# Kernel optimization log

Hardware: AMD Instinct MI355X
Metric: run time of the kernel (lower is better)

Reference implementation:

```python
import jax, jax.numpy as jnp
import numpy as np

B, L, D, N, H = 4, 1024, 1024, 16, 64  # batch, seq, d_model, n_head, d_head
R = 2 * L  # relative position table length
EPS = 1e-5


def setup_inputs() -> dict:
    key = jax.random.key(0)
    ks = jax.random.split(key, 16)
    s = D ** -0.5
    q = jax.random.normal(ks[0], (B, L, D), jnp.float32)
    k = jax.random.normal(ks[1], (B, L, D), jnp.float32)
    v = jax.random.normal(ks[2], (B, L, D), jnp.float32)
    pos_encodings = jax.random.normal(ks[3], (R, D), jnp.float32)
    padding = jax.random.randint(ks[4], (B, 1, 1, L), 0, 2).astype(bool)
    q_w = jax.random.normal(ks[5], (D, N, H), jnp.float32) * s
    k_w = jax.random.normal(ks[6], (D, N, H), jnp.float32) * s
    k_b = jnp.zeros((N, H), jnp.float32)
    v_w = jax.random.normal(ks[7], (D, N, H), jnp.float32) * s
    v_b = jnp.zeros((N, H), jnp.float32)
    r_w_bias = jax.random.normal(ks[8], (N, 1, H), jnp.float32) * 0.02
    r_r_bias = jax.random.normal(ks[9], (N, 1, H), jnp.float32) * 0.02
    r_kernel = jax.random.normal(ks[10], (N, D, H), jnp.float32) * s
    post_w = jax.random.normal(ks[11], (N, H, D), jnp.float32) * (N * H) ** -0.5
    post_b = jnp.zeros((D,), jnp.float32)
    ln_g = jnp.ones((D,), jnp.float32)
    ln_b = jnp.zeros((D,), jnp.float32)
    return dict(q=q, k=k, v=v, pos_encodings=pos_encodings, padding=padding,
                q_w=q_w, k_w=k_w, k_b=k_b, v_w=v_w, v_b=v_b,
                r_w_bias=r_w_bias, r_r_bias=r_r_bias, r_kernel=r_kernel,
                post_w=post_w, post_b=post_b, ln_g=ln_g, ln_b=ln_b)


def _funnel_attention(q, k, v, pos_encodings, padding, q_w, k_w, k_b, v_w, v_b,
                      r_w_bias, r_r_bias, r_kernel, post_w, post_b, ln_g, ln_b):
    input_q = q
    d_head = q_w.shape[-1]
    scale = d_head ** -0.5
    # head projections, laid out [b, n, l, h]
    qh = jnp.einsum('bld,dnh->bnlh', q, q_w)
    kh = jnp.einsum('bld,dnh->bnlh', k, k_w) + k_b[None, :, None, :]
    vh = jnp.einsum('bld,dnh->bnlh', v, v_w) + v_b[None, :, None, :]
    # content term with r_w_bias
    attn_score = jnp.einsum('bnlh,bnmh->bnlm', qh + r_w_bias[None], kh) * scale
    # relative-position term (rel_shift)
    r = jnp.einsum('rd,ndh->nrh', pos_encodings, r_kernel)  # [n, R, h]
    pos = jnp.einsum('bnlh,nrh->bnlr', qh + r_r_bias[None], r) * scale  # [b,n,L,R]
    b, n, q_len, r_len = pos.shape
    k_len = kh.shape[-2]
    shift = 1 + (q_len != k_len)
    pos = pos.reshape(b, n, r_len, q_len)
    pos = pos[:, :, shift:, :]
    pos = pos.reshape(b, n, q_len, r_len - shift)[..., :k_len]
    attn_score = attn_score + pos
    # key padding mask
    attn_score = attn_score - 1e6 * padding.astype(attn_score.dtype)
    attn_dist = jax.nn.softmax(attn_score, axis=-1)
    out = jnp.einsum('bnlm,bnmh->bnlh', attn_dist, vh)
    attn_out = jnp.einsum('bnlh,nhd->bld', out, post_w) + post_b
    x = input_q + attn_out
    mu = jnp.mean(x, axis=-1, keepdims=True)
    var = jnp.mean(jnp.square(x - mu), axis=-1, keepdims=True)
    return (x - mu) * jax.lax.rsqrt(var + EPS) * ln_g + ln_b


def reference(q, k, v, pos_encodings, padding, q_w, k_w, k_b, v_w, v_b,
              r_w_bias, r_r_bias, r_kernel, post_w, post_b, ln_g, ln_b):
    return _funnel_attention(q, k, v, pos_encodings, padding, q_w, k_w, k_b,
                             v_w, v_b, r_w_bias, r_r_bias, r_kernel,
                             post_w, post_b, ln_g, ln_b)
```

## Files before the change

### kernel.cpp

```cpp
#include <hip/hip_runtime.h>
#include <hip/hip_bf16.h>

#define Bb 4
#define Ls 1024
#define Dd 1024
#define Nn 16
#define Hh 64
#define Rr 2048

typedef __attribute__((ext_vector_type(8))) short short8;
typedef __attribute__((ext_vector_type(4))) short short4v;
typedef __attribute__((ext_vector_type(4))) float f32x4;

__device__ __forceinline__ float bf2f(short s) {
    union { unsigned u; float f; } c;
    c.u = ((unsigned)(unsigned short)s) << 16;
    return c.f;
}
__device__ __forceinline__ short f2bf(float f) {
    __hip_bfloat16 h = __float2bfloat16(f);
    return *reinterpret_cast<short*>(&h);
}

__device__ __forceinline__ void gld16(const void* g, void* l) {
    __builtin_amdgcn_global_load_lds(
        (const __attribute__((address_space(1))) unsigned int*)g,
        (__attribute__((address_space(3))) unsigned int*)l, 16, 0, 0);
}

struct CopyDesc {
    const float* src[4];
    short* dst[4];
    int n[4];
};

__global__ __launch_bounds__(256) void f2bf_multi(CopyDesc cd) {
    const int z = blockIdx.y;
    const int base = (blockIdx.x * 256 + threadIdx.x) * 8;
    if (base >= cd.n[z]) return;
    const float* s = cd.src[z] + base;
    const float4 a = *(const float4*)s;
    const float4 b = *(const float4*)(s + 4);
    short8 o;
    o[0] = f2bf(a.x); o[1] = f2bf(a.y); o[2] = f2bf(a.z); o[3] = f2bf(a.w);
    o[4] = f2bf(b.x); o[5] = f2bf(b.y); o[6] = f2bf(b.z); o[7] = f2bf(b.w);
    *(short8*)(cd.dst[z] + base) = o;
}

struct TransDesc {
    const float* src[4];
    short* dst[4];
};

__global__ __launch_bounds__(256) void transpose_all(
    TransDesc td, const float* __restrict__ rker, short* __restrict__ rkT)
{
    const int z = blockIdx.z;
    const float* in; short* out; int C, R;
    if (z < 4) {
        in = td.src[z]; out = td.dst[z]; C = 1024; R = 1024;
    } else {
        if (blockIdx.x != 0) return;
        in  = rker + (long)(z - 4) * 1024 * 64;
        out = rkT  + (long)(z - 4) * 64 * 1024;
        C = 64; R = 1024;
    }
    const int r0 = blockIdx.y * 64, c0 = blockIdx.x * 64;
    __shared__ float T[64][65];
    const int t = threadIdx.x;
    const int rr = t >> 4, c4 = (t & 15) * 4;
#pragma unroll
    for (int p = 0; p < 4; ++p) {
        const float4 v = *(const float4*)&in[(long)(r0 + p * 16 + rr) * C + c0 + c4];
        T[p * 16 + rr][c4 + 0] = v.x;
        T[p * 16 + rr][c4 + 1] = v.y;
        T[p * 16 + rr][c4 + 2] = v.z;
        T[p * 16 + rr][c4 + 3] = v.w;
    }
    __syncthreads();
#pragma unroll
    for (int p = 0; p < 4; ++p) {
        const int j = p * 16 + (t >> 4);
        const int d4 = (t & 15) * 4;
        short4v o;
#pragma unroll
        for (int u = 0; u < 4; ++u) o[u] = f2bf(T[d4 + u][j]);
        *(short4v*)&out[(long)(c0 + j) * R + r0 + d4] = o;
    }
}

__global__ __launch_bounds__(256) void gemm_bt(
    const short* __restrict__ A, int lda, long aStride,
    const short* __restrict__ Bt, int ldb, long bStride,
    const float* __restrict__ bias,
    const float* __restrict__ kb, const float* __restrict__ vb,
    const float* __restrict__ residual, int ldr,
    void* __restrict__ Cv, int ldc, long cStride, int out_bf16, int K, int zsplit)
{
    const int bid   = (int)blockIdx.x;
    const int chunk = (int)gridDim.x >> 3;
    const int work  = (bid & 7) * chunk + (bid >> 3);
    int z, r;
    if (work < zsplit) { z = work >> 8; r = work & 255; }
    else               { z = 3;         r = work - zsplit; }
    const int by = r >> 3;
    const int bx = r & 7;

    A  += (long)z * aStride;
    Bt += (long)z * bStride;

    const int row0 = by * 128;
    const int col0 = bx * 128;

    __shared__ short As[128 * 32];
    __shared__ short Bs[128 * 32];

    const int tid  = threadIdx.x;
    const int w    = tid >> 6;
    const int lane = tid & 63;
    const int quad = lane >> 4;
    const int ln16 = lane & 15;
    const int wr   = (w >> 1) * 64;
    const int wc   = (w & 1) * 64;

    f32x4 acc[4][4];
#pragma unroll
    for (int a = 0; a < 4; ++a)
#pragma unroll
        for (int b = 0; b < 4; ++b) acc[a][b] = (f32x4){0.f, 0.f, 0.f, 0.f};

    const int srow = w * 16 + (lane >> 2);
    const int scol = (lane & 3) * 8;
    const short* gA = A  + (long)(row0 + srow) * lda + scol;
    const short* gB = Bt + (long)(col0 + srow) * ldb + scol;
    short* lA0 = As + w * 512;
    short* lB0 = Bs + w * 512;

    for (int k0 = 0; k0 < K; k0 += 32) {
        __syncthreads();
        gld16(gA + k0,                  lA0);
        gld16(gA + k0 + (long)64 * lda, lA0 + 2048);
        gld16(gB + k0,                  lB0);
        gld16(gB + k0 + (long)64 * ldb, lB0 + 2048);
        __syncthreads();

        short8 af[4], bfr[4];
#pragma unroll
        for (int tm = 0; tm < 4; ++tm)
            af[tm] = *(const short8*)&As[(wr + tm * 16 + ln16) * 32 + quad * 8];
#pragma unroll
        for (int tn = 0; tn < 4; ++tn)
            bfr[tn] = *(const short8*)&Bs[(wc + tn * 16 + ln16) * 32 + quad * 8];
#pragma unroll
        for (int tm = 0; tm < 4; ++tm)
#pragma unroll
            for (int tn = 0; tn < 4; ++tn)
                acc[tm][tn] = __builtin_amdgcn_mfma_f32_16x16x32_bf16(
                    af[tm], bfr[tn], acc[tm][tn], 0, 0, 0);
    }

    const float* bz = bias;
    if (z == 1) bz = kb;
    else if (z == 2) bz = vb;

    float bv[4];
#pragma unroll
    for (int tn = 0; tn < 4; ++tn)
        bv[tn] = bz ? bz[col0 + wc + tn * 16 + ln16] : 0.f;

    short* Cb = (short*)Cv + (long)z * cStride;
    float* Cf = (float*)Cv + (long)z * cStride;
#pragma unroll
    for (int tm = 0; tm < 4; ++tm) {
#pragma unroll
        for (int r2 = 0; r2 < 4; ++r2) {
            const long row = row0 + wr + tm * 16 + quad * 4 + r2;
#pragma unroll
            for (int tn = 0; tn < 4; ++tn) {
                const int col = col0 + wc + tn * 16 + ln16;
                float val = acc[tm][tn][r2] + bv[tn];
                if (residual) val += residual[row * (long)ldr + col];
                if (out_bf16) Cb[row * (long)ldc + col] = f2bf(val);
                else          Cf[row * (long)ldc + col] = val;
            }
        }
    }
}

#define SCALE_L2E 0.18033688f

__global__ __launch_bounds__(256, 2) void attn_mfma(
    const short* __restrict__ qh, const short* __restrict__ kh,
    const short* __restrict__ vh, const short* __restrict__ rS,
    const int* __restrict__ padding, const float* __restrict__ rwb,
    const float* __restrict__ rrb, short* __restrict__ ao)
{
    const int bid   = (int)blockIdx.x;
    const int chunk = (int)gridDim.x >> 3;
    const int work  = (bid & 7) * chunk + (bid >> 3);
    const int lt = work & 7;
    const int n  = (work >> 3) & 15;
    const int b  = work >> 7;

    const int l0 = lt * 128;
    const int tid  = threadIdx.x;
    const int w    = tid >> 6;
    const int lane = tid & 63;
    const int quad = lane >> 4;
    const int ln16 = lane & 15;
    const int qb   = w * 32;

    __shared__ __align__(16) short ks[64 * 64];
    __shared__ __align__(16) short rsb[192 * 64];
    __shared__ __align__(16) short vsT[64][72];
    __shared__ __align__(16) short psm[4][16][72];
    __shared__ float padsAll[Ls];

    for (int i = tid; i < Ls; i += 256) {
        const float mask = -1.0e6f * (float)padding[b * Ls + i];
        padsAll[i] = (mask - 16.0f) * 1.44269504f;
    }

    short8 qwf[2][2], qrf[2][2];
#pragma unroll
    for (int qt = 0; qt < 2; ++qt) {
        const long rowoff =
            ((long)(b * Ls + l0 + qb + qt * 16 + ln16)) * (Nn * Hh) + n * Hh;
#pragma unroll
        for (int c = 0; c < 2; ++c) {
            const int kb2 = c * 32 + quad * 8;
            short8 qv = *(const short8*)(qh + rowoff + kb2);
#pragma unroll
            for (int j = 0; j < 8; ++j) {
                float qf = bf2f(qv[j]);
                qwf[qt][c][j] = f2bf(qf + rwb[n * Hh + kb2 + j]);
                qrf[qt][c][j] = f2bf(qf + rrb[n * Hh + kb2 + j]);
            }
        }
    }

    float lsum[2][4];
    f32x4 accO[2][4];
#pragma unroll
    for (int qt = 0; qt < 2; ++qt)
#pragma unroll
        for (int r = 0; r < 4; ++r) {
            lsum[qt][r] = 0.f;
            accO[qt][r] = (f32x4){0.f, 0.f, 0.f, 0.f};
        }

    const int srow8 = lane >> 3;
    const int sunit = (lane & 7) ^ srow8;
    const int swz   = ln16 & 7;

    const int kp = tid & 31, cq = (tid >> 5) * 8;
    short8 va, vb2;
    {
        const short* vp = vh + ((long)(b * Ls + 2 * kp)) * 1024 + n * 64 + cq;
        va  = *(const short8*)vp;
        vb2 = *(const short8*)(vp + 1024);
    }

    for (int mt = 0; mt < Ls / 64; ++mt) {
        const int m0 = mt * 64;
        __syncthreads();

#pragma unroll
        for (int j = 0; j < 2; ++j) {
            const int c = w * 2 + j;
            gld16(kh + ((long)(b * Ls + m0 + c * 8 + srow8)) * 1024
                     + n * 64 + sunit * 8,
                  ks + c * 512);
        }
        {
            const int blockBase = 897 + m0 - l0;
#pragma unroll
            for (int j = 0; j < 6; ++j) {
                const int c = w * 6 + j;
                int rg = blockBase + c * 8 + srow8;
                rg = rg < 2047 ? rg : 2047;
                gld16(rS + (long)rg * 1024 + n * 64 + sunit * 8,
                      rsb + c * 512);
            }
        }
#pragma unroll
        for (int u = 0; u < 8; ++u) {
            unsigned pk = ((unsigned)(unsigned short)va[u]) |
                          (((unsigned)(unsigned short)vb2[u]) << 16);
            *(unsigned*)&vsT[cq + u][2 * kp] = pk;
        }
        __syncthreads();

        {
            const int mn = (m0 + 64) & (Ls - 1);
            const short* vp = vh + ((long)(b * Ls + mn + 2 * kp)) * 1024 + n * 64 + cq;
            va  = *(const short8*)vp;
            vb2 = *(const short8*)(vp + 1024);
        }

        const int Rbase = (96 - qb) + ln16;
        short8 rfU[6][2];
#pragma unroll
        for (int s = 0; s < 6; ++s) {
#pragma unroll
            for (int c2 = 0; c2 < 2; ++c2) {
                const int unit = (c2 * 4 + quad) ^ swz;
                rfU[s][c2] = *(const short8*)&rsb[(Rbase + s * 16) * 64 + unit * 8];
            }
        }

#pragma unroll
        for (int qt = 0; qt < 2; ++qt) {
            const int off = qt ? 0 : 1;

            f32x4 Sf[4];
#pragma unroll
            for (int t = 0; t < 4; ++t) {
                f32x4 c = (f32x4){0.f, 0.f, 0.f, 0.f};
#pragma unroll
                for (int c2 = 0; c2 < 2; ++c2) {
                    const int unit = (c2 * 4 + quad) ^ swz;
                    short8 kf = *(const short8*)&ks[(t * 16 + ln16) * 64 + unit * 8];
                    c = __builtin_amdgcn_mfma_f32_16x16x32_bf16(qwf[qt][c2], kf, c, 0, 0, 0);
                }
                Sf[t] = c;
            }
            f32x4 Prf[5];
#pragma unroll
            for (int t = 0; t < 5; ++t) {
                f32x4 c = (f32x4){0.f, 0.f, 0.f, 0.f};
                c = __builtin_amdgcn_mfma_f32_16x16x32_bf16(qrf[qt][0], rfU[t + off][0], c, 0, 0, 0);
                c = __builtin_amdgcn_mfma_f32_16x16x32_bf16(qrf[qt][1], rfU[t + off][1], c, 0, 0, 0);
                Prf[t] = c;
            }
            const float mb0 = padsAll[m0 + ln16];
            const float mb1 = padsAll[m0 + 16 + ln16];
            const float mb2 = padsAll[m0 + 32 + ln16];
            const float mb3 = padsAll[m0 + 48 + ln16];
#pragma unroll
            for (int r = 0; r < 4; ++r) {
                const int row = quad * 4 + r;
                const int u = ln16 - row + 15;
                const int srcLane = (quad << 4) | (u & 15);
                const float s0 = __shfl(Prf[0][r], srcLane, 64);
                const float s1 = __shfl(Prf[1][r], srcLane, 64);
                const float s2 = __shfl(Prf[2][r], srcLane, 64);
                const float s3 = __shfl(Prf[3][r], srcLane, 64);
                const float s4 = __shfl(Prf[4][r], srcLane, 64);
                const bool hi = (u >= 16);
                const float p0 = __builtin_amdgcn_exp2f(
                    fmaf(Sf[0][r] + (hi ? s1 : s0), SCALE_L2E, mb0));
                const float p1 = __builtin_amdgcn_exp2f(
                    fmaf(Sf[1][r] + (hi ? s2 : s1), SCALE_L2E, mb1));
                const float p2 = __builtin_amdgcn_exp2f(
                    fmaf(Sf[2][r] + (hi ? s3 : s2), SCALE_L2E, mb2));
                const float p3 = __builtin_amdgcn_exp2f(
                    fmaf(Sf[3][r] + (hi ? s4 : s3), SCALE_L2E, mb3));
                lsum[qt][r] += (p0 + p1) + (p2 + p3);
                psm[w][row][ln16]      = f2bf(p0);
                psm[w][row][16 + ln16] = f2bf(p1);
                psm[w][row][32 + ln16] = f2bf(p2);
                psm[w][row][48 + ln16] = f2bf(p3);
            }

            short8 pA[2];
#pragma unroll
            for (int c2 = 0; c2 < 2; ++c2)
                pA[c2] = *(short8*)&psm[w][ln16][c2 * 32 + quad * 8];
#pragma unroll
            for (int t = 0; t < 4; ++t) {
                f32x4 c = accO[qt][t];
#pragma unroll
                for (int c2 = 0; c2 < 2; ++c2) {
                    short8 vf = *(short8*)&vsT[t * 16 + ln16][c2 * 32 + quad * 8];
                    c = __builtin_amdgcn_mfma_f32_16x16x32_bf16(pA[c2], vf, c, 0, 0, 0);
                }
                accO[qt][t] = c;
            }
        }
    }

#pragma unroll
    for (int qt = 0; qt < 2; ++qt) {
#pragma unroll
        for (int r = 0; r < 4; ++r) {
            float v = lsum[qt][r];
#pragma unroll
            for (int of = 1; of < 16; of <<= 1) v += __shfl_xor(v, of, 64);
            lsum[qt][r] = 1.f / v;
        }
#pragma unroll
        for (int t = 0; t < 4; ++t)
#pragma unroll
            for (int r = 0; r < 4; ++r)
                psm[w][quad * 4 + r][t * 16 + ln16] =
                    f2bf(accO[qt][t][r] * lsum[qt][(unsigned)r]);
#pragma unroll
        for (int p = 0; p < 2; ++p) {
            const int c = lane + p * 64;
            const int row = c >> 3, cq2 = (c & 7) * 8;
            const long grow = (long)(b * Ls + l0 + qb + qt * 16 + row);
            *(short8*)(ao + grow * 1024 + n * 64 + cq2) = *(short8*)&psm[w][row][cq2];
        }
    }
}

__global__ __launch_bounds__(256) void ln_kernel(
    float* x, const float* __restrict__ g, const float* __restrict__ bb)
{
    const int row = blockIdx.x;
    const int tid = threadIdx.x;
    float4 v = ((const float4*)(x + (long)row * Dd))[tid];
    float s  = v.x + v.y + v.z + v.w;
    float sq = v.x * v.x + v.y * v.y + v.z * v.z + v.w * v.w;
#pragma unroll
    for (int off = 32; off; off >>= 1) {
        s  += __shfl_down(s, off, 64);
        sq += __shfl_down(sq, off, 64);
    }
    __shared__ float ws_s[4], ws_q[4];
    __shared__ float s_mu, s_rstd;
    const int wave = tid >> 6, lane = tid & 63;
    if (lane == 0) { ws_s[wave] = s; ws_q[wave] = sq; }
    __syncthreads();
    if (tid == 0) {
        const float ts = ws_s[0] + ws_s[1] + ws_s[2] + ws_s[3];
        const float tq = ws_q[0] + ws_q[1] + ws_q[2] + ws_q[3];
        const float mu = ts / (float)Dd;
        const float var = tq / (float)Dd - mu * mu;
        s_mu = mu;
        s_rstd = rsqrtf(var + 1e-5f);
    }
    __syncthreads();
    const float mu = s_mu, rstd = s_rstd;
    const float4 gv = ((const float4*)g)[tid];
    const float4 bv = ((const float4*)bb)[tid];
    float4 o;
    o.x = (v.x - mu) * rstd * gv.x + bv.x;
    o.y = (v.y - mu) * rstd * gv.y + bv.y;
    o.z = (v.z - mu) * rstd * gv.z + bv.z;
    o.w = (v.w - mu) * rstd * gv.w + bv.w;
    ((float4*)(x + (long)row * Dd))[tid] = o;
}

extern "C" void kernel_launch(void* const* d_in, const int* in_sizes, int n_in,
                              void* d_out, int out_size, void* d_ws, size_t ws_size,
                              hipStream_t stream) {
    const float* q      = (const float*)d_in[0];
    const float* k      = (const float*)d_in[1];
    const float* v      = (const float*)d_in[2];
    const float* posenc = (const float*)d_in[3];
    const int*   pad    = (const int*)  d_in[4];
    const float* q_w    = (const float*)d_in[5];
    const float* k_w    = (const float*)d_in[6];
    const float* k_b    = (const float*)d_in[7];
    const float* v_w    = (const float*)d_in[8];
    const float* v_b    = (const float*)d_in[9];
    const float* rwb    = (const float*)d_in[10];
    const float* rrb    = (const float*)d_in[11];
    const float* r_ker  = (const float*)d_in[12];
    const float* post_w = (const float*)d_in[13];
    const float* post_b = (const float*)d_in[14];
    const float* ln_g   = (const float*)d_in[15];
    const float* ln_b   = (const float*)d_in[16];
    float* out = (float*)d_out;

    const long M1 = 1L << 20;
    short* ws = (short*)d_ws;
    short* xq   = ws;
    short* xk   = ws + 4 * M1;
    short* xv   = ws + 8 * M1;
    short* pe   = ws + 12 * M1;
    short* wT   = ws + 14 * M1;
    short* rkT  = ws + 17 * M1;
    short* pwT  = ws + 18 * M1;
    short* qh   = ws + 19 * M1;
    short* kh   = ws + 23 * M1;
    short* vh   = ws + 27 * M1;
    short* rS   = ws + 31 * M1;
    short* ao   = xq;

    const dim3 blk(256);

    CopyDesc cd;
    cd.src[0] = q;      cd.dst[0] = xq;  cd.n[0] = 4 * (int)M1;
    cd.src[1] = k;      cd.dst[1] = xk;  cd.n[1] = 4 * (int)M1;
    cd.src[2] = v;      cd.dst[2] = xv;  cd.n[2] = 4 * (int)M1;
    cd.src[3] = posenc; cd.dst[3] = pe;  cd.n[3] = 2 * (int)M1;
    f2bf_multi<<<dim3(2048, 4), blk, 0, stream>>>(cd);

    TransDesc td;
    td.src[0] = q_w;    td.dst[0] = wT;
    td.src[1] = k_w;    td.dst[1] = wT + M1;
    td.src[2] = v_w;    td.dst[2] = wT + 2 * M1;
    td.src[3] = post_w; td.dst[3] = pwT;
    transpose_all<<<dim3(16, 16, 20), blk, 0, stream>>>(td, r_ker, rkT);

    gemm_bt<<<dim3(896), blk, 0, stream>>>(
        xq, 1024, 4 * M1, wT, 1024, M1, nullptr, k_b, v_b,
        nullptr, 0, qh, 1024, 4 * M1, 1, 1024, 768);

    attn_mfma<<<dim3(512), blk, 0, stream>>>(
        qh, kh, vh, rS, pad, rwb, rrb, ao);

    gemm_bt<<<dim3(256), blk, 0, stream>>>(
        ao, 1024, 0, pwT, 1024, 0, post_b, nullptr, nullptr,
        q, 1024, out, 1024, 0, 0, 1024, 1 << 30);

    ln_kernel<<<dim3(Bb * Ls), blk, 0, stream>>>(out, ln_g, ln_b);
}
```

Before: 319.5 us.

## Halve attention query tile to 64 rows, bitmask padding, raise occupancy

The attention kernel now processes 64 query rows per block (16 per wave) instead of 128, doubling the grid to 1024 blocks and raising the launch-bounds occupancy hint from 2 to 3. The padding mask is packed into a 32-word ballot bitmask in shared memory rather than a 1024-float table, and the relative-position staging buffer shrinks from 192 to 128 rows. MFMA sections are wrapped in s_setprio to favour matrix issue. The aim is more resident waves to hide latency, at the cost of loading K, V and R tiles twice as often per query row.

Result: no change. 324.8 us (+1.7%).

```diff
diff --git a/kernel.cpp b/kernel.cpp
--- a/kernel.cpp
+++ b/kernel.cpp
@@ -189,7 +189,7 @@
 
 #define SCALE_L2E 0.18033688f
 
-__global__ __launch_bounds__(256, 2) void attn_mfma(
+__global__ __launch_bounds__(256, 3) void attn_mfma(
     const short* __restrict__ qh, const short* __restrict__ kh,
     const short* __restrict__ vh, const short* __restrict__ rS,
     const int* __restrict__ padding, const float* __restrict__ rwb,
@@ -198,34 +198,38 @@
     const int bid   = (int)blockIdx.x;
     const int chunk = (int)gridDim.x >> 3;
     const int work  = (bid & 7) * chunk + (bid >> 3);
-    const int lt = work & 7;
-    const int n  = (work >> 3) & 15;
-    const int b  = work >> 7;
-
-    const int l0 = lt * 128;
+    const int lt = work & 15;
+    const int n  = (work >> 4) & 15;
+    const int b  = work >> 8;
+
+    const int l0 = lt * 64;
     const int tid  = threadIdx.x;
     const int w    = tid >> 6;
     const int lane = tid & 63;
     const int quad = lane >> 4;
     const int ln16 = lane & 15;
-    const int qb   = w * 32;
 
     __shared__ __align__(16) short ks[64 * 64];
-    __shared__ __align__(16) short rsb[192 * 64];
+    __shared__ __align__(16) short rsb[128 * 64];
     __shared__ __align__(16) short vsT[64][72];
     __shared__ __align__(16) short psm[4][16][72];
-    __shared__ float padsAll[Ls];
-
-    for (int i = tid; i < Ls; i += 256) {
-        const float mask = -1.0e6f * (float)padding[b * Ls + i];
-        padsAll[i] = (mask - 16.0f) * 1.44269504f;
-    }
-
-    short8 qwf[2][2], qrf[2][2];
-#pragma unroll
-    for (int qt = 0; qt < 2; ++qt) {
+    __shared__ unsigned padw[32];
+
+#pragma unroll
+    for (int j = 0; j < 4; ++j) {
+        const int g = w + 4 * j;
+        const unsigned long long m =
+            __ballot(padding[b * Ls + g * 64 + lane] != 0);
+        if (lane == 0) {
+            padw[2 * g]     = (unsigned)m;
+            padw[2 * g + 1] = (unsigned)(m >> 32);
+        }
+    }
+
+    short8 qwf[2], qrf[2];
+    {
         const long rowoff =
-            ((long)(b * Ls + l0 + qb + qt * 16 + ln16)) * (Nn * Hh) + n * Hh;
+            ((long)(b * Ls + l0 + w * 16 + ln16)) * (Nn * Hh) + n * Hh;
 #pragma unroll
         for (int c = 0; c < 2; ++c) {
             const int kb2 = c * 32 + quad * 8;
@@ -233,21 +237,19 @@
 #pragma unroll
             for (int j = 0; j < 8; ++j) {
                 float qf = bf2f(qv[j]);
-                qwf[qt][c][j] = f2bf(qf + rwb[n * Hh + kb2 + j]);
-                qrf[qt][c][j] = f2bf(qf + rrb[n * Hh + kb2 + j]);
+                qwf[c][j] = f2bf(qf + rwb[n * Hh + kb2 + j]);
+                qrf[c][j] = f2bf(qf + rrb[n * Hh + kb2 + j]);
             }
         }
     }
 
-    float lsum[2][4];
-    f32x4 accO[2][4];
-#pragma unroll
-    for (int qt = 0; qt < 2; ++qt)
-#pragma unroll
-        for (int r = 0; r < 4; ++r) {
-            lsum[qt][r] = 0.f;
-            accO[qt][r] = (f32x4){0.f, 0.f, 0.f, 0.f};
-        }
+    float lsum[4];
+    f32x4 accO[4];
+#pragma unroll
+    for (int r = 0; r < 4; ++r) {
+        lsum[r] = 0.f;
+        accO[r] = (f32x4){0.f, 0.f, 0.f, 0.f};
+    }
 
     const int srow8 = lane >> 3;
     const int sunit = (lane & 7) ^ srow8;
@@ -273,10 +275,10 @@
                   ks + c * 512);
         }
         {
-            const int blockBase = 897 + m0 - l0;
-#pragma unroll
-            for (int j = 0; j < 6; ++j) {
-                const int c = w * 6 + j;
+            const int blockBase = 961 + m0 - l0;
+#pragma unroll
+            for (int j = 0; j < 4; ++j) {
+                const int c = w * 4 + j;
                 int rg = blockBase + c * 8 + srow8;
                 rg = rg < 2047 ? rg : 2047;
                 gld16(rS + (long)rg * 1024 + n * 64 + sunit * 8,
@@ -298,10 +300,10 @@
             vb2 = *(const short8*)(vp + 1024);
         }
 
-        const int Rbase = (96 - qb) + ln16;
-        short8 rfU[6][2];
-#pragma unroll
-        for (int s = 0; s < 6; ++s) {
+        const int Rbase = 48 - 16 * w + ln16;
+        short8 rfU[5][2];
+#pragma unroll
+        for (int s = 0; s < 5; ++s) {
 #pragma unroll
             for (int c2 = 0; c2 < 2; ++c2) {
                 const int unit = (c2 * 4 + quad) ^ swz;
@@ -309,99 +311,99 @@
             }
         }
 
-#pragma unroll
-        for (int qt = 0; qt < 2; ++qt) {
-            const int off = qt ? 0 : 1;
-
-            f32x4 Sf[4];
-#pragma unroll
-            for (int t = 0; t < 4; ++t) {
-                f32x4 c = (f32x4){0.f, 0.f, 0.f, 0.f};
-#pragma unroll
-                for (int c2 = 0; c2 < 2; ++c2) {
-                    const int unit = (c2 * 4 + quad) ^ swz;
-                    short8 kf = *(const short8*)&ks[(t * 16 + ln16) * 64 + unit * 8];
-                    c = __builtin_amdgcn_mfma_f32_16x16x32_bf16(qwf[qt][c2], kf, c, 0, 0, 0);
-                }
-                Sf[t] = c;
+        __builtin_amdgcn_s_setprio(1);
+        f32x4 Sf[4];
+#pragma unroll
+        for (int t = 0; t < 4; ++t) {
+            f32x4 c = (f32x4){0.f, 0.f, 0.f, 0.f};
+#pragma unroll
+            for (int c2 = 0; c2 < 2; ++c2) {
+                const int unit = (c2 * 4 + quad) ^ swz;
+                short8 kf = *(const short8*)&ks[(t * 16 + ln16) * 64 + unit * 8];
+                c = __builtin_amdgcn_mfma_f32_16x16x32_bf16(qwf[c2], kf, c, 0, 0, 0);
             }
-            f32x4 Prf[5];
-#pragma unroll
-            for (int t = 0; t < 5; ++t) {
-                f32x4 c = (f32x4){0.f, 0.f, 0.f, 0.f};
-                c = __builtin_amdgcn_mfma_f32_16x16x32_bf16(qrf[qt][0], rfU[t + off][0], c, 0, 0, 0);
-                c = __builtin_amdgcn_mfma_f32_16x16x32_bf16(qrf[qt][1], rfU[t + off][1], c, 0, 0, 0);
-                Prf[t] = c;
+            Sf[t] = c;
+        }
+        f32x4 Prf[5];
+#pragma unroll
+        for (int t = 0; t < 5; ++t) {
+            f32x4 c = (f32x4){0.f, 0.f, 0.f, 0.f};
+            c = __builtin_amdgcn_mfma_f32_16x16x32_bf16(qrf[0], rfU[t][0], c, 0, 0, 0);
+            c = __builtin_amdgcn_mfma_f32_16x16x32_bf16(qrf[1], rfU[t][1], c, 0, 0, 0);
+            Prf[t] = c;
+        }
+        __builtin_amdgcn_s_setprio(0);
+
+        const unsigned w0 = padw[(m0 >> 5)];
+        const unsigned w1 = padw[(m0 >> 5) + 1];
+        const float mbc = -16.0f * 1.44269504f;
+        const float mb0 = ((w0 >> ln16) & 1)        ? -1.0e7f : mbc;
+        const float mb1 = ((w0 >> (16 + ln16)) & 1) ? -1.0e7f : mbc;
+        const float mb2 = ((w1 >> ln16) & 1)        ? -1.0e7f : mbc;
+        const float mb3 = ((w1 >> (16 + ln16)) & 1) ? -1.0e7f : mbc;
+#pragma unroll
+        for (int r = 0; r < 4; ++r) {
+            const int row = quad * 4 + r;
+            const int u = ln16 - row + 15;
+            const int srcLane = (quad << 4) | (u & 15);
+            const float s0 = __shfl(Prf[0][r], srcLane, 64);
+            const float s1 = __shfl(Prf[1][r], srcLane, 64);
+            const float s2 = __shfl(Prf[2][r], srcLane, 64);
+            const float s3 = __shfl(Prf[3][r], srcLane, 64);
+            const float s4 = __shfl(Prf[4][r], srcLane, 64);
+            const bool hi = (u >= 16);
+            const float p0 = __builtin_amdgcn_exp2f(
+                fmaf(Sf[0][r] + (hi ? s1 : s0), SCALE_L2E, mb0));
+            const float p1 = __builtin_amdgcn_exp2f(
+                fmaf(Sf[1][r] + (hi ? s2 : s1), SCALE_L2E, mb1));
+            const float p2 = __builtin_amdgcn_exp2f(
+                fmaf(Sf[2][r] + (hi ? s3 : s2), SCALE_L2E, mb2));
+            const float p3 = __builtin_amdgcn_exp2f(
+                fmaf(Sf[3][r] + (hi ? s4 : s3), SCALE_L2E, mb3));
+            lsum[r] += (p0 + p1) + (p2 + p3);
+            psm[w][row][ln16]      = f2bf(p0);
+            psm[w][row][16 + ln16] = f2bf(p1);
+            psm[w][row][32 + ln16] = f2bf(p2);
+            psm[w][row][48 + ln16] = f2bf(p3);
+        }
+
+        short8 pA[2];
+#pragma unroll
+        for (int c2 = 0; c2 < 2; ++c2)
+            pA[c2] = *(short8*)&psm[w][ln16][c2 * 32 + quad * 8];
+        __builtin_amdgcn_s_setprio(1);
+#pragma unroll
+        for (int t = 0; t < 4; ++t) {
+            f32x4 c = accO[t];
+#pragma unroll
+            for (int c2 = 0; c2 < 2; ++c2) {
+                short8 vf = *(short8*)&vsT[t * 16 + ln16][c2 * 32 + quad * 8];
+                c = __builtin_amdgcn_mfma_f32_16x16x32_bf16(pA[c2], vf, c, 0, 0, 0);
             }
-            const float mb0 = padsAll[m0 + ln16];
-            const float mb1 = padsAll[m0 + 16 + ln16];
-            const float mb2 = padsAll[m0 + 32 + ln16];
-            const float mb3 = padsAll[m0 + 48 + ln16];
-#pragma unroll
-            for (int r = 0; r < 4; ++r) {
-                const int row = quad * 4 + r;
-                const int u = ln16 - row + 15;
-                const int srcLane = (quad << 4) | (u & 15);
-                const float s0 = __shfl(Prf[0][r], srcLane, 64);
-                const float s1 = __shfl(Prf[1][r], srcLane, 64);
-                const float s2 = __shfl(Prf[2][r], srcLane, 64);
-                const float s3 = __shfl(Prf[3][r], srcLane, 64);
-                const float s4 = __shfl(Prf[4][r], srcLane, 64);
-                const bool hi = (u >= 16);
-                const float p0 = __builtin_amdgcn_exp2f(
-                    fmaf(Sf[0][r] + (hi ? s1 : s0), SCALE_L2E, mb0));
-                const float p1 = __builtin_amdgcn_exp2f(
-                    fmaf(Sf[1][r] + (hi ? s2 : s1), SCALE_L2E, mb1));
-                const float p2 = __builtin_amdgcn_exp2f(
-                    fmaf(Sf[2][r] + (hi ? s3 : s2), SCALE_L2E, mb2));
-                const float p3 = __builtin_amdgcn_exp2f(
-                    fmaf(Sf[3][r] + (hi ? s4 : s3), SCALE_L2E, mb3));
-                lsum[qt][r] += (p0 + p1) + (p2 + p3);
-                psm[w][row][ln16]      = f2bf(p0);
-                psm[w][row][16 + ln16] = f2bf(p1);
-                psm[w][row][32 + ln16] = f2bf(p2);
-                psm[w][row][48 + ln16] = f2bf(p3);
-            }
-
-            short8 pA[2];
-#pragma unroll
-            for (int c2 = 0; c2 < 2; ++c2)
-                pA[c2] = *(short8*)&psm[w][ln16][c2 * 32 + quad * 8];
-#pragma unroll
-            for (int t = 0; t < 4; ++t) {
-                f32x4 c = accO[qt][t];
-#pragma unroll
-                for (int c2 = 0; c2 < 2; ++c2) {
-                    short8 vf = *(short8*)&vsT[t * 16 + ln16][c2 * 32 + quad * 8];
-                    c = __builtin_amdgcn_mfma_f32_16x16x32_bf16(pA[c2], vf, c, 0, 0, 0);
-                }
-                accO[qt][t] = c;
-            }
-        }
-    }
-
-#pragma unroll
-    for (int qt = 0; qt < 2; ++qt) {
-#pragma unroll
-        for (int r = 0; r < 4; ++r) {
-            float v = lsum[qt][r];
-#pragma unroll
-            for (int of = 1; of < 16; of <<= 1) v += __shfl_xor(v, of, 64);
-            lsum[qt][r] = 1.f / v;
-        }
-#pragma unroll
-        for (int t = 0; t < 4; ++t)
-#pragma unroll
-            for (int r = 0; r < 4; ++r)
-                psm[w][quad * 4 + r][t * 16 + ln16] =
-                    f2bf(accO[qt][t][r] * lsum[qt][(unsigned)r]);
-#pragma unroll
-        for (int p = 0; p < 2; ++p) {
-            const int c = lane + p * 64;
-            const int row = c >> 3, cq2 = (c & 7) * 8;
-            const long grow = (long)(b * Ls + l0 + qb + qt * 16 + row);
-            *(short8*)(ao + grow * 1024 + n * 64 + cq2) = *(short8*)&psm[w][row][cq2];
-        }
+            accO[t] = c;
+        }
+        __builtin_amdgcn_s_setprio(0);
+    }
+
+#pragma unroll
+    for (int r = 0; r < 4; ++r) {
+        float v = lsum[r];
+#pragma unroll
+        for (int of = 1; of < 16; of <<= 1) v += __shfl_xor(v, of, 64);
+        lsum[r] = 1.f / v;
+    }
+#pragma unroll
+    for (int t = 0; t < 4; ++t)
+#pragma unroll
+        for (int r = 0; r < 4; ++r)
+            psm[w][quad * 4 + r][t * 16 + ln16] =
+                f2bf(accO[t][r] * lsum[(unsigned)r]);
+#pragma unroll
+    for (int p = 0; p < 2; ++p) {
+        const int c = lane + p * 64;
+        const int row = c >> 3, cq2 = (c & 7) * 8;
+        const long grow = (long)(b * Ls + l0 + w * 16 + row);
+        *(short8*)(ao + grow * 1024 + n * 64 + cq2) = *(short8*)&psm[w][row][cq2];
     }
 }
 
@@ -500,7 +502,7 @@
         xq, 1024, 4 * M1, wT, 1024, M1, nullptr, k_b, v_b,
         nullptr, 0, qh, 1024, 4 * M1, 1, 1024, 768);
 
-    attn_mfma<<<dim3(512), blk, 0, stream>>>(
+    attn_mfma<<<dim3(1024), blk, 0, stream>>>(
         qh, kh, vh, rS, pad, rwb, rrb, ao);
 
     gemm_bt<<<dim3(256), blk, 0, stream>>>(
```

## Interleave q-tiles in attention loop, bitmask padding, permute P/V layout, add setprio

Applied to the files above, without the earlier changes.

The attention inner loop now handles both 16-row query tiles together, so each K and V fragment is loaded from LDS once and reused across both tiles. The key padding mask is packed into a per-block bitmask built with ballot, replacing the float table in shared memory. The P and V^T staging layouts are permuted so P can be written as packed 4-element stores, and MFMA sections are wrapped in s_setprio. The cost is higher register pressure from keeping both tiles' score fragments live at once, plus a larger psm buffer.

Measured after the change: 307.6 us. -3.7%, faster.

```diff
diff --git a/kernel.cpp b/kernel.cpp
--- a/kernel.cpp
+++ b/kernel.cpp
@@ -213,12 +213,18 @@
     __shared__ __align__(16) short ks[64 * 64];
     __shared__ __align__(16) short rsb[192 * 64];
     __shared__ __align__(16) short vsT[64][72];
-    __shared__ __align__(16) short psm[4][16][72];
-    __shared__ float padsAll[Ls];
-
-    for (int i = tid; i < Ls; i += 256) {
-        const float mask = -1.0e6f * (float)padding[b * Ls + i];
-        padsAll[i] = (mask - 16.0f) * 1.44269504f;
+    __shared__ __align__(16) short psm[4][2][16][72];
+    __shared__ unsigned padw[32];
+
+#pragma unroll
+    for (int j = 0; j < 4; ++j) {
+        const int g = w + 4 * j;
+        const unsigned long long m =
+            __ballot(padding[b * Ls + g * 64 + lane] != 0);
+        if (lane == 0) {
+            padw[2 * g]     = (unsigned)m;
+            padw[2 * g + 1] = (unsigned)(m >> 32);
+        }
     }
 
     short8 qwf[2][2], qrf[2][2];
@@ -253,12 +259,15 @@
     const int sunit = (lane & 7) ^ srow8;
     const int swz   = ln16 & 7;
 
-    const int kp = tid & 31, cq = (tid >> 5) * 8;
+    const int s5  = tid & 31;
+    const int kp2 = (s5 & 15) + ((s5 >> 4) << 5);
+    const int kcb = 4 * (s5 & 15) + 2 * (s5 >> 4);
+    const int cq  = (tid >> 5) * 8;
     short8 va, vb2;
     {
-        const short* vp = vh + ((long)(b * Ls + 2 * kp)) * 1024 + n * 64 + cq;
+        const short* vp = vh + ((long)(b * Ls + kp2)) * 1024 + n * 64 + cq;
         va  = *(const short8*)vp;
-        vb2 = *(const short8*)(vp + 1024);
+        vb2 = *(const short8*)(vp + 16 * 1024);
     }
 
     for (int mt = 0; mt < Ls / 64; ++mt) {
@@ -287,15 +296,15 @@
         for (int u = 0; u < 8; ++u) {
             unsigned pk = ((unsigned)(unsigned short)va[u]) |
                           (((unsigned)(unsigned short)vb2[u]) << 16);
-            *(unsigned*)&vsT[cq + u][2 * kp] = pk;
+            *(unsigned*)&vsT[cq + u][kcb] = pk;
         }
         __syncthreads();
 
         {
             const int mn = (m0 + 64) & (Ls - 1);
-            const short* vp = vh + ((long)(b * Ls + mn + 2 * kp)) * 1024 + n * 64 + cq;
+            const short* vp = vh + ((long)(b * Ls + mn + kp2)) * 1024 + n * 64 + cq;
             va  = *(const short8*)vp;
-            vb2 = *(const short8*)(vp + 1024);
+            vb2 = *(const short8*)(vp + 16 * 1024);
         }
 
         const int Rbase = (96 - qb) + ln16;
@@ -309,75 +318,95 @@
             }
         }
 
-#pragma unroll
-        for (int qt = 0; qt < 2; ++qt) {
-            const int off = qt ? 0 : 1;
-
-            f32x4 Sf[4];
-#pragma unroll
-            for (int t = 0; t < 4; ++t) {
+        __builtin_amdgcn_s_setprio(1);
+        f32x4 Sf[2][4];
+#pragma unroll
+        for (int t = 0; t < 4; ++t) {
+            short8 kf0, kf1;
+            {
+                const int u0 = (0 * 4 + quad) ^ swz;
+                const int u1 = (1 * 4 + quad) ^ swz;
+                kf0 = *(const short8*)&ks[(t * 16 + ln16) * 64 + u0 * 8];
+                kf1 = *(const short8*)&ks[(t * 16 + ln16) * 64 + u1 * 8];
+            }
+#pragma unroll
+            for (int qt = 0; qt < 2; ++qt) {
                 f32x4 c = (f32x4){0.f, 0.f, 0.f, 0.f};
-#pragma unroll
-                for (int c2 = 0; c2 < 2; ++c2) {
-                    const int unit = (c2 * 4 + quad) ^ swz;
-                    short8 kf = *(const short8*)&ks[(t * 16 + ln16) * 64 + unit * 8];
-                    c = __builtin_amdgcn_mfma_f32_16x16x32_bf16(qwf[qt][c2], kf, c, 0, 0, 0);
-                }
-                Sf[t] = c;
-            }
-            f32x4 Prf[5];
-#pragma unroll
-            for (int t = 0; t < 5; ++t) {
+                c = __builtin_amdgcn_mfma_f32_16x16x32_bf16(qwf[qt][0], kf0, c, 0, 0, 0);
+                c = __builtin_amdgcn_mfma_f32_16x16x32_bf16(qwf[qt][1], kf1, c, 0, 0, 0);
+                Sf[qt][t] = c;
+            }
+        }
+        f32x4 Prf[2][5];
+#pragma unroll
+        for (int t = 0; t < 5; ++t) {
+#pragma unroll
+            for (int qt = 0; qt < 2; ++qt) {
+                const int off = qt ? 0 : 1;
                 f32x4 c = (f32x4){0.f, 0.f, 0.f, 0.f};
                 c = __builtin_amdgcn_mfma_f32_16x16x32_bf16(qrf[qt][0], rfU[t + off][0], c, 0, 0, 0);
                 c = __builtin_amdgcn_mfma_f32_16x16x32_bf16(qrf[qt][1], rfU[t + off][1], c, 0, 0, 0);
-                Prf[t] = c;
-            }
-            const float mb0 = padsAll[m0 + ln16];
-            const float mb1 = padsAll[m0 + 16 + ln16];
-            const float mb2 = padsAll[m0 + 32 + ln16];
-            const float mb3 = padsAll[m0 + 48 + ln16];
+                Prf[qt][t] = c;
+            }
+        }
+        __builtin_amdgcn_s_setprio(0);
+
+        const unsigned w0 = padw[(m0 >> 5)];
+        const unsigned w1 = padw[(m0 >> 5) + 1];
+        const float mbc = -16.0f * 1.44269504f;
+        const float mb0 = ((w0 >> ln16) & 1)        ? -1.0e7f : mbc;
+        const float mb1 = ((w0 >> (16 + ln16)) & 1) ? -1.0e7f : mbc;
+        const float mb2 = ((w1 >> ln16) & 1)        ? -1.0e7f : mbc;
+        const float mb3 = ((w1 >> (16 + ln16)) & 1) ? -1.0e7f : mbc;
+#pragma unroll
+        for (int qt = 0; qt < 2; ++qt) {
 #pragma unroll
             for (int r = 0; r < 4; ++r) {
                 const int row = quad * 4 + r;
                 const int u = ln16 - row + 15;
                 const int srcLane = (quad << 4) | (u & 15);
-                const float s0 = __shfl(Prf[0][r], srcLane, 64);
-                const float s1 = __shfl(Prf[1][r], srcLane, 64);
-                const float s2 = __shfl(Prf[2][r], srcLane, 64);
-                const float s3 = __shfl(Prf[3][r], srcLane, 64);
-                const float s4 = __shfl(Prf[4][r], srcLane, 64);
+                const float s0 = __shfl(Prf[qt][0][r], srcLane, 64);
+                const float s1 = __shfl(Prf[qt][1][r], srcLane, 64);
+                const float s2 = __shfl(Prf[qt][2][r], srcLane, 64);
+                const float s3 = __shfl(Prf[qt][3][r], srcLane, 64);
+                const float s4 = __shfl(Prf[qt][4][r], srcLane, 64);
                 const bool hi = (u >= 16);
                 const float p0 = __builtin_amdgcn_exp2f(
-                    fmaf(Sf[0][r] + (hi ? s1 : s0), SCALE_L2E, mb0));
+                    fmaf(Sf[qt][0][r] + (hi ? s1 : s0), SCALE_L2E, mb0));
                 const float p1 = __builtin_amdgcn_exp2f(
-                    fmaf(Sf[1][r] + (hi ? s2 : s1), SCALE_L2E, mb1));
+                    fmaf(Sf[qt][1][r] + (hi ? s2 : s1), SCALE_L2E, mb1));
                 const float p2 = __builtin_amdgcn_exp2f(
-                    fmaf(Sf[2][r] + (hi ? s3 : s2), SCALE_L2E, mb2));
+                    fmaf(Sf[qt][2][r] + (hi ? s3 : s2), SCALE_L2E, mb2));
                 const float p3 = __builtin_amdgcn_exp2f(
-                    fmaf(Sf[3][r] + (hi ? s4 : s3), SCALE_L2E, mb3));
+                    fmaf(Sf[qt][3][r] + (hi ? s4 : s3), SCALE_L2E, mb3));
                 lsum[qt][r] += (p0 + p1) + (p2 + p3);
-                psm[w][row][ln16]      = f2bf(p0);
-                psm[w][row][16 + ln16] = f2bf(p1);
-                psm[w][row][32 + ln16] = f2bf(p2);
-                psm[w][row][48 + ln16] = f2bf(p3);
-            }
-
-            short8 pA[2];
+                short4v pk;
+                pk[0] = f2bf(p0); pk[1] = f2bf(p1);
+                pk[2] = f2bf(p2); pk[3] = f2bf(p3);
+                *(short4v*)&psm[w][qt][row][ln16 * 4] = pk;
+            }
+        }
+
+        short8 pA[2][2];
+#pragma unroll
+        for (int qt = 0; qt < 2; ++qt)
 #pragma unroll
             for (int c2 = 0; c2 < 2; ++c2)
-                pA[c2] = *(short8*)&psm[w][ln16][c2 * 32 + quad * 8];
-#pragma unroll
-            for (int t = 0; t < 4; ++t) {
+                pA[qt][c2] = *(short8*)&psm[w][qt][ln16][c2 * 32 + quad * 8];
+        __builtin_amdgcn_s_setprio(1);
+#pragma unroll
+        for (int t = 0; t < 4; ++t) {
+            short8 vf0 = *(short8*)&vsT[t * 16 + ln16][quad * 8];
+            short8 vf1 = *(short8*)&vsT[t * 16 + ln16][32 + quad * 8];
+#pragma unroll
+            for (int qt = 0; qt < 2; ++qt) {
                 f32x4 c = accO[qt][t];
-#pragma unroll
-                for (int c2 = 0; c2 < 2; ++c2) {
-                    short8 vf = *(short8*)&vsT[t * 16 + ln16][c2 * 32 + quad * 8];
-                    c = __builtin_amdgcn_mfma_f32_16x16x32_bf16(pA[c2], vf, c, 0, 0, 0);
-                }
+                c = __builtin_amdgcn_mfma_f32_16x16x32_bf16(pA[qt][0], vf0, c, 0, 0, 0);
+                c = __builtin_amdgcn_mfma_f32_16x16x32_bf16(pA[qt][1], vf1, c, 0, 0, 0);
                 accO[qt][t] = c;
             }
         }
+        __builtin_amdgcn_s_setprio(0);
     }
 
 #pragma unroll
@@ -393,14 +422,14 @@
         for (int t = 0; t < 4; ++t)
 #pragma unroll
             for (int r = 0; r < 4; ++r)
-                psm[w][quad * 4 + r][t * 16 + ln16] =
+                psm[w][qt][quad * 4 + r][t * 16 + ln16] =
                     f2bf(accO[qt][t][r] * lsum[qt][(unsigned)r]);
 #pragma unroll
         for (int p = 0; p < 2; ++p) {
             const int c = lane + p * 64;
             const int row = c >> 3, cq2 = (c & 7) * 8;
             const long grow = (long)(b * Ls + l0 + qb + qt * 16 + row);
-            *(short8*)(ao + grow * 1024 + n * 64 + cq2) = *(short8*)&psm[w][row][cq2];
+            *(short8*)(ao + grow * 1024 + n * 64 + cq2) = *(short8*)&psm[w][qt][row][cq2];
         }
     }
 }
```
